# Optimization experiments

Measured on AMD Instinct MI355X. Metric: run time of the kernel, lower is better.

Reference implementation:

```python
import jax, jax.numpy as jnp
import numpy as np
from itertools import permutations

NUM_LAYERS = 3
K = 5  # fixed node degree -> every Hungarian sub-problem is 5x5
# one-hot permutation tensor: P1H[p, r, c] = 1 iff permutation p assigns row r -> col c
PERMS = np.array(list(permutations(range(K))), dtype=np.int32)          # [120, K]
P1H = (PERMS[:, :, None] == np.arange(K)[None, None, :]).astype(np.float32)  # [120, K, K]


def _mlp(x, W1, b1, W2, b2):
    # 2-layer MLP with ReLU (repo's MLP(in, hid, out, 2))
    return jax.nn.relu(x @ W1 + b1) @ W2 + b2


def _sinkhorn(src, itera):
    s = jax.nn.softmax(src, axis=1)  # row-max subtraction is built in
    for i in range(itera):
        s = s / jnp.sum(s, axis=i % 2, keepdims=True)
    return jnp.nan_to_num(s)


def _masked_softmax(src):
    s1 = jnp.nan_to_num(jax.nn.softmax(src, axis=1))
    s2 = jnp.nan_to_num(jax.nn.softmax(src, axis=0))
    return (s1 + s2) * 0.5


def setup_inputs() -> dict:
    key = jax.random.key(0)
    ks = jax.random.split(key, 12)
    n1 = n2 = 1024
    hid = 64
    adj1 = jax.random.randint(ks[0], (n1, K), 0, n1)
    adj2 = jax.random.randint(ks[1], (n2, K), 0, n2)
    # adjacency matrices consistent with the neighbor lists
    G1 = jnp.zeros((n1, n1), jnp.float32).at[jnp.arange(n1)[:, None], adj1].set(1.0)
    G2 = jnp.zeros((n2, n2), jnp.float32).at[jnp.arange(n2)[:, None], adj2].set(1.0)
    s = 0.1
    return {
        'G1': G1, 'G2': G2, 'adj1': adj1, 'adj2': adj2,
        'ro_W1': jax.random.normal(ks[2], (NUM_LAYERS, 1, hid), jnp.float32) * s,
        'ro_b1': jax.random.normal(ks[3], (NUM_LAYERS, hid), jnp.float32) * s,
        'ro_W2': jax.random.normal(ks[4], (NUM_LAYERS, hid, 1), jnp.float32) * s,
        'ro_b2': jax.random.normal(ks[5], (NUM_LAYERS, 1), jnp.float32) * s,
        'fin_W1': jax.random.normal(ks[6], (1, hid), jnp.float32) * s,
        'fin_b1': jax.random.normal(ks[7], (hid,), jnp.float32) * s,
        'fin_W2': jax.random.normal(ks[8], (hid, 1), jnp.float32) * s,
        'fin_b2': jax.random.normal(ks[9], (1,), jnp.float32) * s,
    }


def reference(G1, G2, adj1, adj2, ro_W1, ro_b1, ro_W2, ro_b2, fin_W1, fin_b1, fin_W2, fin_b2):
    n1 = G1.shape[0]
    n2 = G2.shape[0]
    d1 = jnp.sum(G1, axis=1)
    d2 = jnp.sum(G2, axis=1)
    ttheta = jnp.mean(d1)
    # S[i, j, 0] = -|d1[i] - d2[j]|
    S = -jnp.abs(d1[:, None] - d2[None, :])[..., None]  # [n1, n2, 1]
    p1h = jnp.asarray(P1H)
    for li in range(NUM_LAYERS):
        Wn = _sinkhorn(_mlp(S / ttheta, ro_W1[li], ro_b1[li], ro_W2[li], ro_b2[li]).squeeze(-1), 5)
        W = jnp.log(Wn * (n1 * 1.5))
        W = jnp.where(jnp.isneginf(W), jnp.float32(-1e12), W)
        W = jnp.where(jnp.isposinf(W), jnp.float32(1e12), W)
        Wd = jax.lax.stop_gradient(W)  # matches W.detach().numpy()
        # small[a, b, r, c] = Wd[adj1[a, r], adj2[b, c]]  -> [n1, n2, K, K]
        small = jnp.transpose(Wd[adj1][:, :, adj2], (0, 2, 1, 3))
        # exact linear_sum_assignment(-small): maximize sum over the K! permutations
        scores = jnp.einsum('abrc,prc->abp', small, p1h)  # [n1, n2, 120]
        X1 = jnp.max(scores, axis=-1)                      # [n1, n2]
        S = X1[..., None]
    out = _masked_softmax(_mlp(S, fin_W1, fin_b1, fin_W2, fin_b2).squeeze(-1))
    return out
```

## Files before the change

### kernel.cpp

```cpp
#include <hip/hip_runtime.h>
#include <math.h>

#define N 1024
#define NB 256
#define KD 5
#define SL 8
#define NT 126
#define MAGIC 0x13572468
#define FSTRIDE 32
#define FREGION (NB * FSTRIDE + FSTRIDE)


__device__ __forceinline__ float load_sc(const float* p){
  return __hip_atomic_load(p, __ATOMIC_RELAXED, __HIP_MEMORY_SCOPE_AGENT);
}
__device__ __forceinline__ void store_sc(float* p, float v){
  __hip_atomic_store(p, v, __ATOMIC_RELAXED, __HIP_MEMORY_SCOPE_AGENT);
}
__device__ __forceinline__ int load_sci(const int* p){
  return __hip_atomic_load(p, __ATOMIC_RELAXED, __HIP_MEMORY_SCOPE_AGENT);
}
__device__ __forceinline__ void store_sci(int* p, int v){
  __hip_atomic_store(p, v, __ATOMIC_RELAXED, __HIP_MEMORY_SCOPE_AGENT);
}

__device__ __forceinline__ void gbarS(int* flg){
  __builtin_amdgcn_s_waitcnt(0);
  __syncthreads();
  const int t = threadIdx.x, B = blockIdx.x;
  int* go = flg + NB * FSTRIDE;
  if (B == 0){
    if (t > 0 && t < NB){
      while (load_sci(&flg[t * FSTRIDE]) != MAGIC) __builtin_amdgcn_s_sleep(2);
    }
    __syncthreads();
    if (t == 0) store_sci(go, MAGIC);
  } else {
    if (t == 0){
      store_sci(&flg[B * FSTRIDE], MAGIC);
      while (load_sci(go) != MAGIC) __builtin_amdgcn_s_sleep(2);
    }
    __syncthreads();
  }
}

__device__ __forceinline__ float wred_sum(float v){
#pragma unroll
  for (int off = 32; off > 0; off >>= 1) v += __shfl_down(v, off);
  return v;
}
__device__ __forceinline__ void bsum4(float v[4], float* s64){
  float w0 = wred_sum(v[0]), w1 = wred_sum(v[1]), w2 = wred_sum(v[2]), w3 = wred_sum(v[3]);
  __syncthreads();
  int wv = threadIdx.x >> 6;
  if ((threadIdx.x & 63) == 0){ s64[wv*4] = w0; s64[wv*4+1] = w1; s64[wv*4+2] = w2; s64[wv*4+3] = w3; }
  __syncthreads();
  float r0 = 0.f, r1 = 0.f, r2 = 0.f, r3 = 0.f;
#pragma unroll
  for (int i = 0; i < 16; ++i){ r0 += s64[i*4]; r1 += s64[i*4+1]; r2 += s64[i*4+2]; r3 += s64[i*4+3]; }
  v[0] = r0; v[1] = r1; v[2] = r2; v[3] = r3;
}

__device__ __forceinline__ int distinct5(const int* v){
  int c = 0;
#pragma unroll
  for (int r = 0; r < KD; ++r){
    bool dup = false;
#pragma unroll
    for (int s = 0; s < r; ++s) dup = dup || (v[s] == v[r]);
    c += dup ? 0 : 1;
  }
  return c;
}
__device__ __forceinline__ void sort5(int* s){
#pragma unroll
  for (int i = 0; i < 4; ++i)
#pragma unroll
    for (int j = 0; j < 4 - i; ++j){
      int a = s[j], b = s[j+1];
      s[j] = min(a, b); s[j+1] = max(a, b);
    }
}
__device__ __forceinline__ int msrank(const int* c5){
  const int C_[6][5] = { {0,0,0,0,0},
                         {1,1,1,1,1},
                         {1,2,3,4,5},
                         {1,3,6,10,15},
                         {1,4,10,20,35},
                         {1,5,15,35,70} };
  int rank = 0, prev = 0;
#pragma unroll
  for (int i = 0; i < 5; ++i){
    for (int v = prev; v < c5[i]; ++v) rank += C_[5 - v][4 - i];
    prev = c5[i];
  }
  return rank;
}

#define DP5(ACCESS, OUT) {                                        \
  float f[32]; f[0] = 0.f;                                        \
  _Pragma("unroll")                                               \
  for (int r = 0; r < KD; ++r){                                   \
    float tr[KD];                                                 \
    _Pragma("unroll")                                             \
    for (int c = 0; c < KD; ++c) tr[c] = (ACCESS);                \
    _Pragma("unroll")                                             \
    for (int m = 1; m < 32; ++m){                                 \
      if (__popc(m) == r + 1){                                    \
        float best = -3.0e38f;                                    \
        _Pragma("unroll")                                         \
        for (int c = 0; c < KD; ++c)                              \
          if (m & (1 << c)) best = fmaxf(best, f[m ^ (1 << c)] + tr[c]); \
        f[m] = best;                                              \
      }                                                           \
    }                                                             \
  }                                                               \
  OUT = f[31];                                                    \
}

__global__ __launch_bounds__(1024) void
kTable(const int* __restrict__ adj1, const int* __restrict__ adj2,
       const float* __restrict__ roW1, const float* __restrict__ roB1,
       const float* __restrict__ roW2, const float* __restrict__ roB2,
       float* __restrict__ tY1g, float* __restrict__ ttp)
{
  __shared__ unsigned char t2c[NT][5];
  __shared__ int h1[8], h2[8];
  __shared__ float A1[NT], B1[NT];
  __shared__ float sY0[25], slR0[5], slC0[5], stt2[2];
  __shared__ float ux[64], udA[64], udB[64], xs1[64], dA1[64], dB1[64];
  __shared__ float At1[65], Bt1[65], sA0B0[2];
  const int t = threadIdx.x, B = blockIdx.x;
  const float L1536 = logf(1536.0f);

  if (t < 8){ h1[t] = 0; h2[t] = 0; }
#pragma unroll 1
  for (int key = t; key < 3125; key += 1024){
    int d[5]; int k2 = key;
#pragma unroll
    for (int i = 0; i < 5; ++i){ d[i] = k2 % 5; k2 /= 5; }
    if (d[0] <= d[1] && d[1] <= d[2] && d[2] <= d[3] && d[3] <= d[4]){
      int r = msrank(d);
#pragma unroll
      for (int i = 0; i < 5; ++i) t2c[r][i] = (unsigned char)d[i];
    }
  }
  {
    int a2[KD], a1v[KD];
#pragma unroll
    for (int c = 0; c < KD; ++c) a2[c] = adj2[t * KD + c];
#pragma unroll
    for (int r = 0; r < KD; ++r) a1v[r] = adj1[t * KD + r];
    atomicAdd(&h2[distinct5(a2) - 1], 1);
    atomicAdd(&h1[distinct5(a1v) - 1], 1);
  }
  __syncthreads();

  if (t < 64){
    float cnt1[5], cnt2[5];
#pragma unroll
    for (int g = 0; g < 5; ++g){ cnt1[g] = (float)h1[g]; cnt2[g] = (float)h2[g]; }
    float tt = 0.f;
#pragma unroll
    for (int g = 0; g < 5; ++g) tt += (float)(g + 1) * cnt1[g];
    tt *= (1.0f / 1024.0f);
    float tab[5];
#pragma unroll 1
    for (int i = 0; i < 5; ++i){
      float x = -(float)i / tt;
      float acc = roB2[0];
      for (int k = 0; k < 64; ++k){
        float hh = fmaxf(fmaf(x, roW1[k], roB1[k]), 0.f);
        acc = fmaf(hh, roW2[k], acc);
      }
      tab[i] = acc;
    }
    float Ee[5][5];
#pragma unroll
    for (int g = 0; g < 5; ++g)
#pragma unroll
      for (int h = 0; h < 5; ++h) Ee[g][h] = expf(tab[abs(g - h)]);
    float q0[5], C1c[5], q1[5], C2c[5], q2[5], C3c[5];
#pragma unroll
    for (int g = 0; g < 5; ++g){
      float s = 0.f;
#pragma unroll
      for (int h = 0; h < 5; ++h) s += cnt2[h] * Ee[g][h];
      q0[g] = s;
    }
#pragma unroll
    for (int h = 0; h < 5; ++h){
      float s = 0.f;
#pragma unroll
      for (int g = 0; g < 5; ++g) s += cnt1[g] * Ee[g][h] / q0[g];
      C1c[h] = s;
    }
#pragma unroll
    for (int g = 0; g < 5; ++g){
      float s = 0.f;
#pragma unroll
      for (int h = 0; h < 5; ++h) s += cnt2[h] * Ee[g][h] / C1c[h];
      q1[g] = s;
    }
#pragma unroll
    for (int h = 0; h < 5; ++h){
      float s = 0.f;
#pragma unroll
      for (int g = 0; g < 5; ++g) s += cnt1[g] * Ee[g][h] / q1[g];
      C2c[h] = s;
    }
#pragma unroll
    for (int g = 0; g < 5; ++g){
      float s = 0.f;
#pragma unroll
      for (int h = 0; h < 5; ++h) s += cnt2[h] * Ee[g][h] / C2c[h];
      q2[g] = s;
    }
#pragma unroll
    for (int h = 0; h < 5; ++h){
      float s = 0.f;
#pragma unroll
      for (int g = 0; g < 5; ++g) s += cnt1[g] * Ee[g][h] / q2[g];
      C3c[h] = s;
    }
    if (t == 0){
#pragma unroll
      for (int g = 0; g < 5; ++g){
#pragma unroll
        for (int h = 0; h < 5; ++h) sY0[g * 5 + h] = tab[abs(g - h)];
        slR0[g] = -logf(q2[g]);
        slC0[g] = logf(C3c[g]);
      }
      stt2[0] = tt;
    }
  } else if (t < 128){
    int l = t - 64;
    const float* w1g = roW1 + 64;
    const float* b1g = roB1 + 64;
    const float* w2g = roW2 + 64;
    const float* b2g = roB2 + 1;
    float w1 = w1g[l], bb = b1g[l], w2v = w2g[l];
    float xk, sdA, sdB, a0t = 0.f, b0t = 0.f;
    if (w1 != 0.f){
      xk = -bb / w1;
      float dA = w1 * w2v, dB = bb * w2v;
      if (w1 > 0.f){ sdA = dA;  sdB = dB; }
      else         { sdA = -dA; sdB = -dB; a0t = dA; b0t = dB; }
    } else {
      xk = 3.0e38f; sdA = 0.f; sdB = 0.f;
      b0t = fmaxf(bb, 0.f) * w2v;
    }
    ux[l] = xk; udA[l] = sdA; udB[l] = sdB;
    float A0 = wred_sum(a0t);
    float B0 = wred_sum(b0t);
    if (l == 0){ sA0B0[0] = A0; sA0B0[1] = B0 + b2g[0]; }
  }
  __syncthreads();

  if (t < 64){
    float xk = ux[t]; int rank = 0;
    for (int j = 0; j < 64; ++j){
      float xj = ux[j];
      rank += (xj < xk || (xj == xk && j < t)) ? 1 : 0;
    }
    xs1[rank] = ux[t]; dA1[rank] = udA[t]; dB1[rank] = udB[t];
  } else if (t >= 256 && t < 256 + NT){
    int ty = t - 256;
    float sa = 5.0f * L1536, sb = 0.f;
#pragma unroll
    for (int i = 0; i < KD; ++i){
      int cl = t2c[ty][i];
      sa += slR0[cl];
      sb -= slC0[cl];
    }
    A1[ty] = sa; B1[ty] = sb;
  }
  __syncthreads();
  if (t < 65){
    float sa = sA0B0[0], sb = sA0B0[1];
    for (int r = 0; r < t; ++r){ sa += dA1[r]; sb += dB1[r]; }
    At1[t] = sa; Bt1[t] = sb;
  }
  __syncthreads();

  const float tt = stt2[0];
  if (B == 0 && t == 0) ttp[0] = tt;
  if (t < 63){
    int e = B + 256 * t;
    if (e < NT * NT){
      int tau = e / NT, ups = e - tau * NT;
      const unsigned char* G = t2c[tau];
      const unsigned char* H = t2c[ups];
      float D;
      DP5(sY0[(int)G[r] * 5 + (int)H[c]], D);
      float x = (A1[tau] + B1[ups] + D) / tt;
      int seg = 0;
#pragma unroll
      for (int s = 64; s; s >>= 1)
        if (seg + s <= 64 && xs1[seg + s - 1] <= x) seg += s;
      tY1g[e] = fmaf(At1[seg], x, Bt1[seg]);
    }
  }
}

__global__ __launch_bounds__(1024) void
kProd(const int* __restrict__ adj1, const int* __restrict__ adj2,
      const float* __restrict__ w1g, const float* __restrict__ b1g,
      const float* __restrict__ w2g, const float* __restrict__ b2g,
      const float* __restrict__ tY1g, const float* __restrict__ ttp,
      float* __restrict__ t2out, float* __restrict__ C1B)
{
  __shared__ float tY1[NT * NT];
  __shared__ unsigned char sg1[N], sg2[N];
  __shared__ unsigned short st1[N], st2[N];
  __shared__ int cnt1T[NT], cnt2T[NT];
  __shared__ float slR1[NT], slC1[NT];
  __shared__ float vq[NT], vC[NT], vqi[NT], vCi[NT];
  __shared__ float s64[64];
  __shared__ float sAv[4];
  __shared__ float ux[64], udA[64], udB[64], xs2[64], dA2[64], dB2[64];
  __shared__ float At2[65], Bt2[65], sA0B0[2];
  const int t = threadIdx.x, B = blockIdx.x;
  const float L1536 = logf(1536.0f);
  const float tt = ttp[0];

  if (t < NT){ cnt1T[t] = 0; cnt2T[t] = 0; }
#pragma unroll 1
  for (int e = t; e < NT * NT; e += 1024) tY1[e] = tY1g[e];
  int a2[KD], a1v[KD];
#pragma unroll
  for (int c = 0; c < KD; ++c) a2[c] = adj2[t * KD + c];
#pragma unroll
  for (int r = 0; r < KD; ++r) a1v[r] = adj1[t * KD + r];
  sg2[t] = (unsigned char)(distinct5(a2) - 1);
  sg1[t] = (unsigned char)(distinct5(a1v) - 1);
  __syncthreads();

  {
    int c5[KD];
#pragma unroll
    for (int r = 0; r < KD; ++r) c5[r] = sg1[a1v[r]];
    sort5(c5);
    int ty = msrank(c5);
    st1[t] = (unsigned short)ty; atomicAdd(&cnt1T[ty], 1);
  }
  {
    int c5[KD];
#pragma unroll
    for (int c = 0; c < KD; ++c) c5[c] = sg2[a2[c]];
    sort5(c5);
    int ty = msrank(c5);
    st2[t] = (unsigned short)ty; atomicAdd(&cnt2T[ty], 1);
  }
  if (t < 64){
    float w1 = w1g[t], bb = b1g[t], w2v = w2g[t];
    float xk, sdA, sdB, a0t = 0.f, b0t = 0.f;
    if (w1 != 0.f){
      xk = -bb / w1;
      float dA = w1 * w2v, dB = bb * w2v;
      if (w1 > 0.f){ sdA = dA;  sdB = dB; }
      else         { sdA = -dA; sdB = -dB; a0t = dA; b0t = dB; }
    } else {
      xk = 3.0e38f; sdA = 0.f; sdB = 0.f;
      b0t = fmaxf(bb, 0.f) * w2v;
    }
    ux[t] = xk; udA[t] = sdA; udB[t] = sdB;
    float A0 = wred_sum(a0t);
    float B0 = wred_sum(b0t);
    if (t == 0){ sA0B0[0] = A0; sA0B0[1] = B0 + b2g[0]; }
  }
  __syncthreads();
  if (t < 64){
    float xk = ux[t]; int rank = 0;
    for (int j = 0; j < 64; ++j){
      float xj = ux[j];
      rank += (xj < xk || (xj == xk && j < t)) ? 1 : 0;
    }
    xs2[rank] = ux[t]; dA2[rank] = udA[t]; dB2[rank] = udB[t];
  }
  __syncthreads();
  if (t < 65){
    float sa = sA0B0[0], sb = sA0B0[1];
    for (int r = 0; r < t; ++r){ sa += dA2[r]; sb += dB2[r]; }
    At2[t] = sa; Bt2[t] = sb;
  }
  __syncthreads();

  {
    int g = t >> 3, j = t & 7;
    if (g < NT){
      float acc = 0.f;
      for (int u = j; u < NT; u += 8) acc += (float)cnt2T[u] * expf(tY1[g * NT + u]);
      acc += __shfl_down(acc, 4, 8); acc += __shfl_down(acc, 2, 8); acc += __shfl_down(acc, 1, 8);
      if (j == 0){ vq[g] = acc; vqi[g] = 1.0f / acc; }
    }
    __syncthreads();
    if (g < NT){
      float acc = 0.f;
      for (int u = j; u < NT; u += 8) acc += (float)cnt1T[u] * expf(tY1[u * NT + g]) * vqi[u];
      acc += __shfl_down(acc, 4, 8); acc += __shfl_down(acc, 2, 8); acc += __shfl_down(acc, 1, 8);
      if (j == 0){ vC[g] = acc; vCi[g] = 1.0f / acc; }
    }
    __syncthreads();
    if (g < NT){
      float acc = 0.f;
      for (int u = j; u < NT; u += 8) acc += (float)cnt2T[u] * expf(tY1[g * NT + u]) * vCi[u];
      acc += __shfl_down(acc, 4, 8); acc += __shfl_down(acc, 2, 8); acc += __shfl_down(acc, 1, 8);
      if (j == 0){ vq[g] = acc; vqi[g] = 1.0f / acc; }
    }
    __syncthreads();
    if (g < NT){
      float acc = 0.f;
      for (int u = j; u < NT; u += 8) acc += (float)cnt1T[u] * expf(tY1[u * NT + g]) * vqi[u];
      acc += __shfl_down(acc, 4, 8); acc += __shfl_down(acc, 2, 8); acc += __shfl_down(acc, 1, 8);
      if (j == 0){ vC[g] = acc; vCi[g] = 1.0f / acc; }
    }
    __syncthreads();
    if (g < NT){
      float acc = 0.f;
      for (int u = j; u < NT; u += 8) acc += (float)cnt2T[u] * expf(tY1[g * NT + u]) * vCi[u];
      acc += __shfl_down(acc, 4, 8); acc += __shfl_down(acc, 2, 8); acc += __shfl_down(acc, 1, 8);
      if (j == 0){ vq[g] = acc; vqi[g] = 1.0f / acc; }
    }
    __syncthreads();
    if (g < NT){
      float acc = 0.f;
      for (int u = j; u < NT; u += 8) acc += (float)cnt1T[u] * expf(tY1[u * NT + g]) * vqi[u];
      acc += __shfl_down(acc, 4, 8); acc += __shfl_down(acc, 2, 8); acc += __shfl_down(acc, 1, 8);
      if (j == 0) vC[g] = acc;
    }
    __syncthreads();
  }
  if (t < NT){ slR1[t] = -logf(vq[t]); slC1[t] = logf(vC[t]); }
  __syncthreads();

  if (t < 4){
    int a = 4 * B + t;
    float s = 5.0f * L1536;
#pragma unroll
    for (int r = 0; r < KD; ++r) s += slR1[st1[adj1[a * KD + r]]];
    sAv[t] = s;
  }
  int stc[KD];
  float Bv2 = 0.f;
#pragma unroll
  for (int c = 0; c < KD; ++c){ stc[c] = st2[a2[c]]; Bv2 -= slC1[stc[c]]; }
  __syncthreads();

  float y[4];
#pragma unroll 1
  for (int rr = 0; rr < 4; ++rr){
    int str_[KD];
#pragma unroll
    for (int r = 0; r < KD; ++r) str_[r] = st1[adj1[(4 * B + rr) * KD + r]];
    float D;
    DP5(tY1[str_[r] * NT + stc[c]], D);
    float x = (sAv[rr] + Bv2 + D) / tt;
    int seg = 0;
#pragma unroll
    for (int s = 64; s; s >>= 1)
      if (seg + s <= 64 && xs2[seg + s - 1] <= x) seg += s;
    y[rr] = fmaf(At2[seg], x, Bt2[seg]);
  }
  float e4[4], q4[4];
#pragma unroll
  for (int r = 0; r < 4; ++r){ e4[r] = expf(y[r]); q4[r] = e4[r]; }
  bsum4(q4, s64);
  float cp = 0.f;
#pragma unroll
  for (int r = 0; r < 4; ++r){
    t2out[(size_t)(4 * B + r) * N + t] = y[r];
    cp += e4[r] / q4[r];
  }
  atomicAdd(&C1B[(size_t)(B & (SL - 1)) * N + t], cp);
}

__global__ __launch_bounds__(1024) void
kLayerF(const float* __restrict__ tm, const int* __restrict__ adj1, const int* __restrict__ adj2,
        const float* __restrict__ C1B, float* __restrict__ C2B, float* __restrict__ C3B,
        float* __restrict__ CFB, float* __restrict__ Rg,
        const float* __restrict__ w1g, const float* __restrict__ b1g,
        const float* __restrict__ w2g, const float* __restrict__ b2g,
        float* __restrict__ outp,
        int* __restrict__ bar1, int* __restrict__ bar2, int* __restrict__ bar3)
{
  __shared__ __align__(16) float rows20[20][N];
  __shared__ float lc[N];
  __shared__ float s64[64];
  __shared__ float sAv[4];
  __shared__ float ux[64], udA[64], udB[64], xs_s[64], dA_s[64], dB_s[64];
  __shared__ float A_tab[65], B_tab[65], sA0B0[2];
  const int t = threadIdx.x, B = blockIdx.x;

  int a2[KD];
#pragma unroll
  for (int c = 0; c < KD; ++c) a2[c] = adj2[t * KD + c];

  {
    int w = t >> 6, lane = t & 63;
    int seg = w & 3;
    int rbase = w >> 2;
#pragma unroll
    for (int k = 0; k < 5; ++k){
      int r2 = rbase + 4 * k;
      int src = adj1[(4 * B + (r2 / 5)) * KD + (r2 % 5)];
      const float* g = tm + (size_t)src * N + seg * 256 + lane * 4;
      __builtin_amdgcn_global_load_lds(
          (const __attribute__((address_space(1))) unsigned int*)g,
          (__attribute__((address_space(3))) unsigned int*)&rows20[r2][seg * 256],
          16, 0, 0);
    }
  }
  float E[4], q4[4];
#pragma unroll
  for (int r = 0; r < 4; ++r) E[r] = expf(tm[(size_t)(4 * B + r) * N + t]);

  if (t < 64){
    float w1 = w1g[t], bb = b1g[t], w2 = w2g[t];
    float xk, sdA, sdB, a0t = 0.f, b0t = 0.f;
    if (w1 != 0.f){
      xk = -bb / w1;
      float dA = w1 * w2, dB = bb * w2;
      if (w1 > 0.f){ sdA = dA;  sdB = dB; }
      else         { sdA = -dA; sdB = -dB; a0t = dA; b0t = dB; }
    } else {
      xk = 3.0e38f; sdA = 0.f; sdB = 0.f;
      b0t = fmaxf(bb, 0.f) * w2;
    }
    ux[t] = xk; udA[t] = sdA; udB[t] = sdB;
    float A0 = wred_sum(a0t);
    float B0 = wred_sum(b0t);
    if (t == 0){ sA0B0[0] = A0; sA0B0[1] = B0 + b2g[0]; }
  }
  __syncthreads();
  if (t < 64){
    float xk = ux[t]; int rank = 0;
    for (int j = 0; j < 64; ++j){
      float xj = ux[j];
      rank += (xj < xk || (xj == xk && j < t)) ? 1 : 0;
    }
    xs_s[rank] = ux[t]; dA_s[rank] = udA[t]; dB_s[rank] = udB[t];
  }
  __syncthreads();
  if (t < 65){
    float sa = sA0B0[0], sb = sA0B0[1];
    for (int r = 0; r < t; ++r){ sa += dA_s[r]; sb += dB_s[r]; }
    A_tab[t] = sa; B_tab[t] = sb;
  }

  {
    float C = 0.f;
#pragma unroll
    for (int k = 0; k < SL; ++k) C += C1B[(size_t)k * N + t];
    float iC = 1.0f / C;
#pragma unroll
    for (int r = 0; r < 4; ++r) q4[r] = E[r] * iC;
    bsum4(q4, s64);
    float cp = 0.f;
#pragma unroll
    for (int r = 0; r < 4; ++r) cp += E[r] / q4[r];
    atomicAdd(&C2B[(size_t)(B & (SL - 1)) * N + t], cp);
  }

  gbarS(bar1);
  {
    float C = 0.f;
#pragma unroll
    for (int k = 0; k < SL; ++k) C += load_sc(&C2B[(size_t)k * N + t]);
    float iC = 1.0f / C;
#pragma unroll
    for (int r = 0; r < 4; ++r) q4[r] = E[r] * iC;
    bsum4(q4, s64);
    float cp = 0.f;
#pragma unroll
    for (int r = 0; r < 4; ++r) cp += E[r] / q4[r];
    if (t < 4) store_sc(&Rg[4 * B + t], 1.0f / q4[t]);
    atomicAdd(&C3B[(size_t)(B & (SL - 1)) * N + t], cp);
  }

  gbarS(bar2);
  {
    float C = 0.f;
#pragma unroll
    for (int k = 0; k < SL; ++k) C += load_sc(&C3B[(size_t)k * N + t]);
    lc[t] = logf(C);
  }
  if (t >= 64 && t < 68){
    int a = 4 * B + (t - 64);
    float s = 5.0f * logf(1536.0f);
#pragma unroll
    for (int r = 0; r < KD; ++r) s += logf(load_sc(&Rg[adj1[a * KD + r]]));
    sAv[t - 64] = s;
  }
  __syncthreads();

  float Bvl = 0.f;
#pragma unroll
  for (int c = 0; c < KD; ++c) Bvl -= lc[a2[c]];

  float y[4];
#pragma unroll 1
  for (int rr = 0; rr < 4; ++rr){
    float D;
    DP5(rows20[rr * 5 + r][a2[c]], D);
    float x = sAv[rr] + Bvl + D;
    int seg = 0;
#pragma unroll
    for (int s = 64; s; s >>= 1)
      if (seg + s <= 64 && xs_s[seg + s - 1] <= x) seg += s;
    y[rr] = fmaf(A_tab[seg], x, B_tab[seg]);
  }

  float e4[4];
#pragma unroll
  for (int r = 0; r < 4; ++r){ e4[r] = expf(y[r]); q4[r] = e4[r]; }
  bsum4(q4, s64);

  float cp = 0.f;
#pragma unroll
  for (int r = 0; r < 4; ++r) cp += e4[r];
  atomicAdd(&CFB[(size_t)(B & (SL - 1)) * N + t], cp);

  gbarS(bar3);
  float CF = 0.f;
#pragma unroll
  for (int k = 0; k < SL; ++k) CF += load_sc(&CFB[(size_t)k * N + t]);
  float iCF = 1.0f / CF;
#pragma unroll
  for (int r = 0; r < 4; ++r){
    float v = 0.5f * e4[r] * (1.0f / q4[r] + iCF);
    outp[(size_t)(4 * B + r) * N + t] = v;
  }
}

extern "C" void kernel_launch(void* const* d_in, const int* in_sizes, int n_in,
                              void* d_out, int out_size, void* d_ws, size_t ws_size,
                              hipStream_t stream){
  (void)in_sizes; (void)n_in; (void)out_size; (void)ws_size;
  const int*   adj1 = (const int*)d_in[2];
  const int*   adj2 = (const int*)d_in[3];
  const float* roW1 = (const float*)d_in[4];
  const float* roB1 = (const float*)d_in[5];
  const float* roW2 = (const float*)d_in[6];
  const float* roB2 = (const float*)d_in[7];
  const float* fW1  = (const float*)d_in[8];
  const float* fB1  = (const float*)d_in[9];
  const float* fW2  = (const float*)d_in[10];
  const float* fB2  = (const float*)d_in[11];
  float* out = (float*)d_out;

  float* Pp   = (float*)d_ws;
  float* Rg   = Pp + (size_t)4 * SL * N;
  float* ttp  = Rg + N;
  float* tY1g = ttp + 8;
  int*   flg  = (int*)(tY1g + NT * NT);

  kTable<<<NB, 1024, 0, stream>>>(adj1, adj2, roW1, roB1, roW2, roB2, tY1g, ttp);
  kProd<<<NB, 1024, 0, stream>>>(adj1, adj2,
                                 roW1 + 128, roB1 + 128, roW2 + 128, roB2 + 2,
                                 tY1g, ttp, out, Pp);
  kLayerF<<<NB, 1024, 0, stream>>>(out, adj1, adj2,
                                   Pp + (size_t)0 * SL * N, Pp + (size_t)1 * SL * N,
                                   Pp + (size_t)2 * SL * N, Pp + (size_t)3 * SL * N, Rg,
                                   fW1, fB1, fW2, fB2, out,
                                   flg + 0 * FREGION, flg + 1 * FREGION, flg + 2 * FREGION);
}
```

Baseline: 161.9 us.

## Fuse table, product and final-layer kernels into one persistent kernel

Merges the three kernel launches into a single persistent kernel that uses device-wide software barriers between phases and a union of shared memory reused across phases. It removes two launch gaps and the redundant recomputation of degree classes and node types in the second kernel. The async global-to-LDS row gather is replaced by plain coherent loads. The code now relies on all 256 blocks being co-resident and adds two more grid barriers. The flag region now spans five barrier slots, and the workspace layout is unchanged apart from dropping ttp.

```diff
diff --git a/kernel.cpp b/kernel.cpp
--- a/kernel.cpp
+++ b/kernel.cpp
@@ -118,22 +118,82 @@
   OUT = f[31];                                                    \
 }
 
+__device__ __forceinline__ void pwl_build(int t,
+    const float* __restrict__ w1g, const float* __restrict__ b1g,
+    const float* __restrict__ w2g, const float* __restrict__ b2g,
+    float* ux, float* udA, float* udB,
+    float* xss, float* dAs, float* dBs,
+    float* Atb, float* Btb, float* sA0B0)
+{
+  if (t < 64){
+    float w1 = w1g[t], bb = b1g[t], w2v = w2g[t];
+    float xk, sdA, sdB, a0t = 0.f, b0t = 0.f;
+    if (w1 != 0.f){
+      xk = -bb / w1;
+      float dA = w1 * w2v, dB = bb * w2v;
+      if (w1 > 0.f){ sdA = dA;  sdB = dB; }
+      else         { sdA = -dA; sdB = -dB; a0t = dA; b0t = dB; }
+    } else {
+      xk = 3.0e38f; sdA = 0.f; sdB = 0.f;
+      b0t = fmaxf(bb, 0.f) * w2v;
+    }
+    ux[t] = xk; udA[t] = sdA; udB[t] = sdB;
+    float A0 = wred_sum(a0t);
+    float B0 = wred_sum(b0t);
+    if (t == 0){ sA0B0[0] = A0; sA0B0[1] = B0 + b2g[0]; }
+  }
+  __syncthreads();
+  if (t < 64){
+    float xk = ux[t]; int rank = 0;
+    for (int j = 0; j < 64; ++j){
+      float xj = ux[j];
+      rank += (xj < xk || (xj == xk && j < t)) ? 1 : 0;
+    }
+    xss[rank] = ux[t]; dAs[rank] = udA[t]; dBs[rank] = udB[t];
+  }
+  __syncthreads();
+  if (t < 65){
+    float sa = sA0B0[0], sb = sA0B0[1];
+    for (int r = 0; r < t; ++r){ sa += dAs[r]; sb += dBs[r]; }
+    Atb[t] = sa; Btb[t] = sb;
+  }
+  __syncthreads();
+}
+
 __global__ __launch_bounds__(1024) void
-kTable(const int* __restrict__ adj1, const int* __restrict__ adj2,
+kFused(const int* __restrict__ adj1, const int* __restrict__ adj2,
        const float* __restrict__ roW1, const float* __restrict__ roB1,
        const float* __restrict__ roW2, const float* __restrict__ roB2,
-       float* __restrict__ tY1g, float* __restrict__ ttp)
+       const float* __restrict__ fW1, const float* __restrict__ fB1,
+       const float* __restrict__ fW2, const float* __restrict__ fB2,
+       float* __restrict__ tY1g,
+       float* __restrict__ C1B, float* __restrict__ C2B, float* __restrict__ C3B,
+       float* __restrict__ CFB, float* __restrict__ Rg,
+       float* __restrict__ outp,
+       int* __restrict__ flg)
 {
+  __shared__ __align__(16) char uS[20 * N * 4 + N * 4];
+  float* tY1 = (float*)uS;
+  float (*rows20)[N] = (float (*)[N])uS;
+  float* lc = (float*)(uS + 20 * N * 4);
   __shared__ unsigned char t2c[NT][5];
+  __shared__ unsigned char sg1[N], sg2[N];
+  __shared__ unsigned short st1[N], st2[N];
   __shared__ int h1[8], h2[8];
+  __shared__ int cnt1T[NT], cnt2T[NT];
   __shared__ float A1[NT], B1[NT];
   __shared__ float sY0[25], slR0[5], slC0[5], stt2[2];
-  __shared__ float ux[64], udA[64], udB[64], xs1[64], dA1[64], dB1[64];
-  __shared__ float At1[65], Bt1[65], sA0B0[2];
+  __shared__ float slR1[NT], slC1[NT];
+  __shared__ float vq[NT], vC[NT], vqi[NT], vCi[NT];
+  __shared__ float s64[64], sAv[4];
+  __shared__ float ux[64], udA[64], udB[64], xss[64], dAs[64], dBs[64];
+  __shared__ float Atb[65], Btb[65], sA0B0[2];
+
   const int t = threadIdx.x, B = blockIdx.x;
   const float L1536 = logf(1536.0f);
 
   if (t < 8){ h1[t] = 0; h2[t] = 0; }
+  if (t < NT){ cnt1T[t] = 0; cnt2T[t] = 0; }
 #pragma unroll 1
   for (int key = t; key < 3125; key += 1024){
     int d[5]; int k2 = key;
@@ -145,16 +205,35 @@
       for (int i = 0; i < 5; ++i) t2c[r][i] = (unsigned char)d[i];
     }
   }
-  {
-    int a2[KD], a1v[KD];
-#pragma unroll
-    for (int c = 0; c < KD; ++c) a2[c] = adj2[t * KD + c];
-#pragma unroll
-    for (int r = 0; r < KD; ++r) a1v[r] = adj1[t * KD + r];
-    atomicAdd(&h2[distinct5(a2) - 1], 1);
-    atomicAdd(&h1[distinct5(a1v) - 1], 1);
-  }
-  __syncthreads();
+  int a2[KD], a1v[KD];
+#pragma unroll
+  for (int c = 0; c < KD; ++c) a2[c] = adj2[t * KD + c];
+#pragma unroll
+  for (int r = 0; r < KD; ++r) a1v[r] = adj1[t * KD + r];
+  {
+    int c2 = distinct5(a2) - 1, c1 = distinct5(a1v) - 1;
+    sg2[t] = (unsigned char)c2; sg1[t] = (unsigned char)c1;
+    atomicAdd(&h2[c2], 1);
+    atomicAdd(&h1[c1], 1);
+  }
+  __syncthreads();
+
+  {
+    int c5[KD];
+#pragma unroll
+    for (int r = 0; r < KD; ++r) c5[r] = sg1[a1v[r]];
+    sort5(c5);
+    int ty = msrank(c5);
+    st1[t] = (unsigned short)ty; atomicAdd(&cnt1T[ty], 1);
+  }
+  {
+    int c5[KD];
+#pragma unroll
+    for (int c = 0; c < KD; ++c) c5[c] = sg2[a2[c]];
+    sort5(c5);
+    int ty = msrank(c5);
+    st2[t] = (unsigned short)ty; atomicAdd(&cnt2T[ty], 1);
+  }
 
   if (t < 64){
     float cnt1[5], cnt2[5];
@@ -263,7 +342,7 @@
       float xj = ux[j];
       rank += (xj < xk || (xj == xk && j < t)) ? 1 : 0;
     }
-    xs1[rank] = ux[t]; dA1[rank] = udA[t]; dB1[rank] = udB[t];
+    xss[rank] = ux[t]; dAs[rank] = udA[t]; dBs[rank] = udB[t];
   } else if (t >= 256 && t < 256 + NT){
     int ty = t - 256;
     float sa = 5.0f * L1536, sb = 0.f;
@@ -278,13 +357,12 @@
   __syncthreads();
   if (t < 65){
     float sa = sA0B0[0], sb = sA0B0[1];
-    for (int r = 0; r < t; ++r){ sa += dA1[r]; sb += dB1[r]; }
-    At1[t] = sa; Bt1[t] = sb;
+    for (int r = 0; r < t; ++r){ sa += dAs[r]; sb += dBs[r]; }
+    Atb[t] = sa; Btb[t] = sb;
   }
   __syncthreads();
 
   const float tt = stt2[0];
-  if (B == 0 && t == 0) ttp[0] = tt;
   if (t < 63){
     int e = B + 256 * t;
     if (e < NT * NT){
@@ -297,94 +375,18 @@
       int seg = 0;
 #pragma unroll
       for (int s = 64; s; s >>= 1)
-        if (seg + s <= 64 && xs1[seg + s - 1] <= x) seg += s;
-      tY1g[e] = fmaf(At1[seg], x, Bt1[seg]);
-    }
-  }
-}
-
-__global__ __launch_bounds__(1024) void
-kProd(const int* __restrict__ adj1, const int* __restrict__ adj2,
-      const float* __restrict__ w1g, const float* __restrict__ b1g,
-      const float* __restrict__ w2g, const float* __restrict__ b2g,
-      const float* __restrict__ tY1g, const float* __restrict__ ttp,
-      float* __restrict__ t2out, float* __restrict__ C1B)
-{
-  __shared__ float tY1[NT * NT];
-  __shared__ unsigned char sg1[N], sg2[N];
-  __shared__ unsigned short st1[N], st2[N];
-  __shared__ int cnt1T[NT], cnt2T[NT];
-  __shared__ float slR1[NT], slC1[NT];
-  __shared__ float vq[NT], vC[NT], vqi[NT], vCi[NT];
-  __shared__ float s64[64];
-  __shared__ float sAv[4];
-  __shared__ float ux[64], udA[64], udB[64], xs2[64], dA2[64], dB2[64];
-  __shared__ float At2[65], Bt2[65], sA0B0[2];
-  const int t = threadIdx.x, B = blockIdx.x;
-  const float L1536 = logf(1536.0f);
-  const float tt = ttp[0];
-
-  if (t < NT){ cnt1T[t] = 0; cnt2T[t] = 0; }
+        if (seg + s <= 64 && xss[seg + s - 1] <= x) seg += s;
+      store_sc(&tY1g[e], fmaf(Atb[seg], x, Btb[seg]));
+    }
+  }
+
+  gbarS(flg + 0 * FREGION);
+
 #pragma unroll 1
-  for (int e = t; e < NT * NT; e += 1024) tY1[e] = tY1g[e];
-  int a2[KD], a1v[KD];
-#pragma unroll
-  for (int c = 0; c < KD; ++c) a2[c] = adj2[t * KD + c];
-#pragma unroll
-  for (int r = 0; r < KD; ++r) a1v[r] = adj1[t * KD + r];
-  sg2[t] = (unsigned char)(distinct5(a2) - 1);
-  sg1[t] = (unsigned char)(distinct5(a1v) - 1);
-  __syncthreads();
-
-  {
-    int c5[KD];
-#pragma unroll
-    for (int r = 0; r < KD; ++r) c5[r] = sg1[a1v[r]];
-    sort5(c5);
-    int ty = msrank(c5);
-    st1[t] = (unsigned short)ty; atomicAdd(&cnt1T[ty], 1);
-  }
-  {
-    int c5[KD];
-#pragma unroll
-    for (int c = 0; c < KD; ++c) c5[c] = sg2[a2[c]];
-    sort5(c5);
-    int ty = msrank(c5);
-    st2[t] = (unsigned short)ty; atomicAdd(&cnt2T[ty], 1);
-  }
-  if (t < 64){
-    float w1 = w1g[t], bb = b1g[t], w2v = w2g[t];
-    float xk, sdA, sdB, a0t = 0.f, b0t = 0.f;
-    if (w1 != 0.f){
-      xk = -bb / w1;
-      float dA = w1 * w2v, dB = bb * w2v;
-      if (w1 > 0.f){ sdA = dA;  sdB = dB; }
-      else         { sdA = -dA; sdB = -dB; a0t = dA; b0t = dB; }
-    } else {
-      xk = 3.0e38f; sdA = 0.f; sdB = 0.f;
-      b0t = fmaxf(bb, 0.f) * w2v;
-    }
-    ux[t] = xk; udA[t] = sdA; udB[t] = sdB;
-    float A0 = wred_sum(a0t);
-    float B0 = wred_sum(b0t);
-    if (t == 0){ sA0B0[0] = A0; sA0B0[1] = B0 + b2g[0]; }
-  }
-  __syncthreads();
-  if (t < 64){
-    float xk = ux[t]; int rank = 0;
-    for (int j = 0; j < 64; ++j){
-      float xj = ux[j];
-      rank += (xj < xk || (xj == xk && j < t)) ? 1 : 0;
-    }
-    xs2[rank] = ux[t]; dA2[rank] = udA[t]; dB2[rank] = udB[t];
-  }
-  __syncthreads();
-  if (t < 65){
-    float sa = sA0B0[0], sb = sA0B0[1];
-    for (int r = 0; r < t; ++r){ sa += dA2[r]; sb += dB2[r]; }
-    At2[t] = sa; Bt2[t] = sb;
-  }
-  __syncthreads();
+  for (int e = t; e < NT * NT; e += 1024) tY1[e] = load_sc(&tY1g[e]);
+
+  pwl_build(t, roW1 + 128, roB1 + 128, roW2 + 128, roB2 + 2,
+            ux, udA, udB, xss, dAs, dBs, Atb, Btb, sA0B0);
 
   {
     int g = t >> 3, j = t & 7;
@@ -447,7 +449,7 @@
   for (int c = 0; c < KD; ++c){ stc[c] = st2[a2[c]]; Bv2 -= slC1[stc[c]]; }
   __syncthreads();
 
-  float y[4];
+  float y2[4];
 #pragma unroll 1
   for (int rr = 0; rr < 4; ++rr){
     int str_[KD];
@@ -459,99 +461,38 @@
     int seg = 0;
 #pragma unroll
     for (int s = 64; s; s >>= 1)
-      if (seg + s <= 64 && xs2[seg + s - 1] <= x) seg += s;
-    y[rr] = fmaf(At2[seg], x, Bt2[seg]);
-  }
-  float e4[4], q4[4];
-#pragma unroll
-  for (int r = 0; r < 4; ++r){ e4[r] = expf(y[r]); q4[r] = e4[r]; }
+      if (seg + s <= 64 && xss[seg + s - 1] <= x) seg += s;
+    y2[rr] = fmaf(Atb[seg], x, Btb[seg]);
+  }
+  float E[4], q4[4];
+#pragma unroll
+  for (int r = 0; r < 4; ++r){ E[r] = expf(y2[r]); q4[r] = E[r]; }
   bsum4(q4, s64);
-  float cp = 0.f;
-#pragma unroll
-  for (int r = 0; r < 4; ++r){
-    t2out[(size_t)(4 * B + r) * N + t] = y[r];
-    cp += e4[r] / q4[r];
-  }
-  atomicAdd(&C1B[(size_t)(B & (SL - 1)) * N + t], cp);
-}
-
-__global__ __launch_bounds__(1024) void
-kLayerF(const float* __restrict__ tm, const int* __restrict__ adj1, const int* __restrict__ adj2,
-        const float* __restrict__ C1B, float* __restrict__ C2B, float* __restrict__ C3B,
-        float* __restrict__ CFB, float* __restrict__ Rg,
-        const float* __restrict__ w1g, const float* __restrict__ b1g,
-        const float* __restrict__ w2g, const float* __restrict__ b2g,
-        float* __restrict__ outp,
-        int* __restrict__ bar1, int* __restrict__ bar2, int* __restrict__ bar3)
-{
-  __shared__ __align__(16) float rows20[20][N];
-  __shared__ float lc[N];
-  __shared__ float s64[64];
-  __shared__ float sAv[4];
-  __shared__ float ux[64], udA[64], udB[64], xs_s[64], dA_s[64], dB_s[64];
-  __shared__ float A_tab[65], B_tab[65], sA0B0[2];
-  const int t = threadIdx.x, B = blockIdx.x;
-
-  int a2[KD];
-#pragma unroll
-  for (int c = 0; c < KD; ++c) a2[c] = adj2[t * KD + c];
-
-  {
-    int w = t >> 6, lane = t & 63;
-    int seg = w & 3;
-    int rbase = w >> 2;
-#pragma unroll
-    for (int k = 0; k < 5; ++k){
-      int r2 = rbase + 4 * k;
-      int src = adj1[(4 * B + (r2 / 5)) * KD + (r2 % 5)];
-      const float* g = tm + (size_t)src * N + seg * 256 + lane * 4;
-      __builtin_amdgcn_global_load_lds(
-          (const __attribute__((address_space(1))) unsigned int*)g,
-          (__attribute__((address_space(3))) unsigned int*)&rows20[r2][seg * 256],
-          16, 0, 0);
-    }
-  }
-  float E[4], q4[4];
-#pragma unroll
-  for (int r = 0; r < 4; ++r) E[r] = expf(tm[(size_t)(4 * B + r) * N + t]);
-
-  if (t < 64){
-    float w1 = w1g[t], bb = b1g[t], w2 = w2g[t];
-    float xk, sdA, sdB, a0t = 0.f, b0t = 0.f;
-    if (w1 != 0.f){
-      xk = -bb / w1;
-      float dA = w1 * w2, dB = bb * w2;
-      if (w1 > 0.f){ sdA = dA;  sdB = dB; }
-      else         { sdA = -dA; sdB = -dB; a0t = dA; b0t = dB; }
-    } else {
-      xk = 3.0e38f; sdA = 0.f; sdB = 0.f;
-      b0t = fmaxf(bb, 0.f) * w2;
-    }
-    ux[t] = xk; udA[t] = sdA; udB[t] = sdB;
-    float A0 = wred_sum(a0t);
-    float B0 = wred_sum(b0t);
-    if (t == 0){ sA0B0[0] = A0; sA0B0[1] = B0 + b2g[0]; }
-  }
-  __syncthreads();
-  if (t < 64){
-    float xk = ux[t]; int rank = 0;
-    for (int j = 0; j < 64; ++j){
-      float xj = ux[j];
-      rank += (xj < xk || (xj == xk && j < t)) ? 1 : 0;
-    }
-    xs_s[rank] = ux[t]; dA_s[rank] = udA[t]; dB_s[rank] = udB[t];
-  }
-  __syncthreads();
-  if (t < 65){
-    float sa = sA0B0[0], sb = sA0B0[1];
-    for (int r = 0; r < t; ++r){ sa += dA_s[r]; sb += dB_s[r]; }
-    A_tab[t] = sa; B_tab[t] = sb;
-  }
+  {
+    float cp = 0.f;
+#pragma unroll
+    for (int r = 0; r < 4; ++r){
+      store_sc(&outp[(size_t)(4 * B + r) * N + t], y2[r]);
+      cp += E[r] / q4[r];
+    }
+    atomicAdd(&C1B[(size_t)(B & (SL - 1)) * N + t], cp);
+  }
+
+  gbarS(flg + 1 * FREGION);
+
+#pragma unroll
+  for (int k = 0; k < 20; ++k){
+    int src = adj1[(4 * B + (k / 5)) * KD + (k % 5)];
+    rows20[k][t] = load_sc(&outp[(size_t)src * N + t]);
+  }
+
+  pwl_build(t, fW1, fB1, fW2, fB2,
+            ux, udA, udB, xss, dAs, dBs, Atb, Btb, sA0B0);
 
   {
     float C = 0.f;
 #pragma unroll
-    for (int k = 0; k < SL; ++k) C += C1B[(size_t)k * N + t];
+    for (int k = 0; k < SL; ++k) C += load_sc(&C1B[(size_t)k * N + t]);
     float iC = 1.0f / C;
 #pragma unroll
     for (int r = 0; r < 4; ++r) q4[r] = E[r] * iC;
@@ -562,7 +503,7 @@
     atomicAdd(&C2B[(size_t)(B & (SL - 1)) * N + t], cp);
   }
 
-  gbarS(bar1);
+  gbarS(flg + 2 * FREGION);
   {
     float C = 0.f;
 #pragma unroll
@@ -578,7 +519,7 @@
     atomicAdd(&C3B[(size_t)(B & (SL - 1)) * N + t], cp);
   }
 
-  gbarS(bar2);
+  gbarS(flg + 3 * FREGION);
   {
     float C = 0.f;
 #pragma unroll
@@ -607,8 +548,8 @@
     int seg = 0;
 #pragma unroll
     for (int s = 64; s; s >>= 1)
-      if (seg + s <= 64 && xs_s[seg + s - 1] <= x) seg += s;
-    y[rr] = fmaf(A_tab[seg], x, B_tab[seg]);
+      if (seg + s <= 64 && xss[seg + s - 1] <= x) seg += s;
+    y[rr] = fmaf(Atb[seg], x, Btb[seg]);
   }
 
   float e4[4];
@@ -616,12 +557,14 @@
   for (int r = 0; r < 4; ++r){ e4[r] = expf(y[r]); q4[r] = e4[r]; }
   bsum4(q4, s64);
 
-  float cp = 0.f;
-#pragma unroll
-  for (int r = 0; r < 4; ++r) cp += e4[r];
-  atomicAdd(&CFB[(size_t)(B & (SL - 1)) * N + t], cp);
-
-  gbarS(bar3);
+  {
+    float cp = 0.f;
+#pragma unroll
+    for (int r = 0; r < 4; ++r) cp += e4[r];
+    atomicAdd(&CFB[(size_t)(B & (SL - 1)) * N + t], cp);
+  }
+
+  gbarS(flg + 4 * FREGION);
   float CF = 0.f;
 #pragma unroll
   for (int k = 0; k < SL; ++k) CF += load_sc(&CFB[(size_t)k * N + t]);
@@ -651,17 +594,13 @@
 
   float* Pp   = (float*)d_ws;
   float* Rg   = Pp + (size_t)4 * SL * N;
-  float* ttp  = Rg + N;
-  float* tY1g = ttp + 8;
+  float* tY1g = Rg + N;
   int*   flg  = (int*)(tY1g + NT * NT);
 
-  kTable<<<NB, 1024, 0, stream>>>(adj1, adj2, roW1, roB1, roW2, roB2, tY1g, ttp);
-  kProd<<<NB, 1024, 0, stream>>>(adj1, adj2,
-                                 roW1 + 128, roB1 + 128, roW2 + 128, roB2 + 2,
-                                 tY1g, ttp, out, Pp);
-  kLayerF<<<NB, 1024, 0, stream>>>(out, adj1, adj2,
-                                   Pp + (size_t)0 * SL * N, Pp + (size_t)1 * SL * N,
-                                   Pp + (size_t)2 * SL * N, Pp + (size_t)3 * SL * N, Rg,
-                                   fW1, fB1, fW2, fB2, out,
-                                   flg + 0 * FREGION, flg + 1 * FREGION, flg + 2 * FREGION);
-}
+  kFused<<<NB, 1024, 0, stream>>>(adj1, adj2, roW1, roB1, roW2, roB2,
+                                  fW1, fB1, fW2, fB2,
+                                  tY1g,
+                                  Pp + (size_t)0 * SL * N, Pp + (size_t)1 * SL * N,
+                                  Pp + (size_t)2 * SL * N, Pp + (size_t)3 * SL * N,
+                                  Rg, out, flg);
+}
```

Measured after the change: 162.3 us. Within noise of the previous version (+0.2%).
